# Kernel tuning notes

Hardware: AMD Instinct MI355X
Metric: run time of the kernel (lower is better)

Reference implementation:

```python
import jax, jax.numpy as jnp
import numpy as np

B, S, D, H = 16, 512, 768, 8
DK = D // H
MAXREL = 128
VOCAB = 30000


def setup_inputs() -> dict:
    key = jax.random.key(0)
    ks = jax.random.split(key, 20)
    p = lambda i, shape: (jax.random.normal(ks[i], shape, dtype=jnp.float32) * 0.02)
    return {
        "inputs": jax.random.normal(ks[0], (B, S, D), dtype=jnp.float32),
        "tok": jax.random.randint(ks[1], (B, S), 0, VOCAB),
        "seq_lens": S,
        "Wq": p(2, (D, D)), "bq": jnp.zeros((D,), jnp.float32),
        "Wk": p(3, (D, D)), "bk": jnp.zeros((D,), jnp.float32),
        "rel_emb": p(4, (2 * MAXREL + 1, DK)),
        "W0": p(5, (D, D)), "b0": jnp.zeros((D,), jnp.float32),
        "W1": p(6, (D, D)), "b1": jnp.zeros((D,), jnp.float32),
        "scale_w": jnp.ones((2,), jnp.float32) / 2.0,
        "Wf": p(7, (D, D)), "bf": jnp.zeros((D,), jnp.float32),
        "Wfc": p(8, (2 * D, D)), "bfc": jnp.zeros((D,), jnp.float32),
        "Wg": p(9, (D, D)), "bg": jnp.zeros((D,), jnp.float32),
    }


def reference(inputs, tok, seq_lens, Wq, bq, Wk, bk, rel_emb, W0, b0, W1, b1,
              scale_w, Wf, bf, Wfc, bfc, Wg, bg):
    b, s, d = inputs.shape
    h = H
    dk = d // h
    scale = 1.0 / jnp.sqrt(jnp.asarray(dk, inputs.dtype))

    # projections -> (b, h, s, dk)
    q = (inputs @ Wq + bq).reshape(b, s, h, dk).transpose(0, 2, 1, 3)
    k = (inputs @ Wk + bk).reshape(b, s, h, dk).transpose(0, 2, 1, 3)

    scores = jnp.einsum('bhqd,bhkd->bhqk', q, k) * scale

    # relative position bias from head-mean query
    pos = jnp.arange(s)
    dist = jnp.clip(pos[None, :] - pos[:, None], -MAXREL, MAXREL) + MAXREL
    rel = rel_emb[dist]                          # (s, s, dk)
    q_mean = q.mean(axis=1)                      # (b, s, dk)
    rel_scores = jnp.einsum('bqd,qkd->bqk', q_mean, rel) * scale
    scores = scores + rel_scores[:, None]        # broadcast over heads

    key_mask = (tok != 0)[:, None, None, :]      # (b,1,1,s)
    scores = jnp.where(key_mask, scores, jnp.asarray(-1e9, scores.dtype))
    p_attn = jax.nn.softmax(scores, axis=-1)     # (b,h,s,s)

    # head-averaged adjacency with forced self-loops
    adj = p_attn.mean(axis=1)                    # (b,s,s)
    eye = jnp.eye(s, dtype=adj.dtype)
    adj = adj * (1.0 - eye) + eye
    mask_ = (tok != 0).astype(adj.dtype)[:, :seq_lens, None]  # (b,s,1)
    adj = mask_ * adj

    denom = adj.sum(axis=2, keepdims=True) + 1.0

    # dense GCN layers (dropout = identity at inference)
    out = inputs
    feats = []
    for Wl, bl in ((W0, b0), (W1, b1)):
        ax = adj @ out                           # (b,s,d)
        out = jax.nn.relu((ax @ Wl + bl) / denom)
        feats.append(out)

    # multi-scale fusion
    w = jax.nn.softmax(scale_w)
    combined = w[0] * feats[0] + w[1] * feats[1]
    x = combined @ Wf + bf

    # global context gating (pool over full sequence)
    g_avg = x.mean(axis=1)
    g_max = x.max(axis=1)
    gc = jnp.concatenate([g_avg, g_max], axis=-1) @ Wfc + bfc  # (b,d)
    gate = jax.nn.sigmoid(gc @ Wg + bg)                        # (b,d)
    outputs = x + gate[:, None, :] * gc[:, None, :]
    return (outputs, adj)
```

## Files before the change

kernel.cpp:

```cpp
#include <hip/hip_runtime.h>
#include <hip/hip_bf16.h>
#include <math.h>

#define Bc 16
#define Sc 512
#define Dc 768
#define Hc 8
#define DKc 96
#define MAXRELc 128
#define RBLD 384

typedef __attribute__((ext_vector_type(8))) short bf16x8;
typedef __attribute__((ext_vector_type(4))) float f32x4;

static __device__ __forceinline__ unsigned short f2b(float f) {
    __hip_bfloat16 h = __float2bfloat16(f);
    return *(unsigned short*)&h;
}
static __device__ __forceinline__ float b2f(unsigned short u) {
    union { float f; unsigned v; } x;
    x.v = ((unsigned)u) << 16;
    return x.f;
}

static __device__ __forceinline__ long long fl_off(int rowg, int d) {
    const int h = d / 96, rr = d % 96;
    const int ks = rr >> 5, lg = (rr >> 3) & 3, ii = rr & 7;
    return ((((long long)(rowg >> 4) * 8 + h) * 3 + ks) * 4 + lg) * 128 + (rowg & 15) * 8 + ii;
}

#if defined(__has_builtin)
#if __has_builtin(__builtin_amdgcn_global_load_lds)
#define HAS_GLLDS 1
#endif
#endif

#ifdef HAS_GLLDS
typedef __attribute__((address_space(1))) void as1_void;
typedef __attribute__((address_space(3))) void as3_void;
static __device__ __forceinline__ void gl_lds16(const void* g, void* l) {
    __builtin_amdgcn_global_load_lds((as1_void*)(unsigned long long)g,
                                     (as3_void*)(unsigned long long)l, 16, 0, 0);
}
#endif

#define SWS(row, lg) (((((lg) + ((row) >> 1)) & 3)) * 8)

__global__ __launch_bounds__(256) void cvt_bf16_kernel(const float* __restrict__ in,
                                                       unsigned short* __restrict__ out)
{
    const long long idx = ((long long)blockIdx.x * 256 + threadIdx.x) * 8;
    const float4 a = *(const float4*)(in + idx);
    const float4 b = *(const float4*)(in + idx + 4);
    bf16x8 v;
    v[0] = (short)f2b(a.x); v[1] = (short)f2b(a.y); v[2] = (short)f2b(a.z); v[3] = (short)f2b(a.w);
    v[4] = (short)f2b(b.x); v[5] = (short)f2b(b.y); v[6] = (short)f2b(b.z); v[7] = (short)f2b(b.w);
    *(bf16x8*)(out + idx) = v;
}

struct WT5 { const float* s[5]; unsigned short* d[5]; };

__global__ __launch_bounds__(256) void wtrans5_kernel(WT5 p)
{
    const float* W = p.s[blockIdx.z];
    unsigned short* Wt = p.d[blockIdx.z];
    __shared__ float td[64][65];
    const int n0 = blockIdx.x * 64, k0 = blockIdx.y * 64;
    const int t = threadIdx.x, r = t >> 2, c4 = (t & 3) * 16;
#pragma unroll
    for (int j = 0; j < 4; ++j) {
        const float4 v = *(const float4*)(W + (long long)(k0 + r) * Dc + n0 + c4 + j * 4);
        td[r][c4 + j * 4 + 0] = v.x;
        td[r][c4 + j * 4 + 1] = v.y;
        td[r][c4 + j * 4 + 2] = v.z;
        td[r][c4 + j * 4 + 3] = v.w;
    }
    __syncthreads();
    bf16x8 v0, v1;
#pragma unroll
    for (int i = 0; i < 8; ++i) {
        v0[i] = (short)f2b(td[c4 + i][r]);
        v1[i] = (short)f2b(td[c4 + 8 + i][r]);
    }
    unsigned short* dst = Wt + (long long)(n0 + r) * Dc + k0 + c4;
    *(bf16x8*)dst = v0;
    *(bf16x8*)(dst + 8) = v1;
}

__global__ __launch_bounds__(256) void catbias_kernel(const float* __restrict__ a,
                                                      const float* __restrict__ b,
                                                      float* __restrict__ o)
{
    const int i = blockIdx.x * 256 + threadIdx.x;
    o[i] = (i < Dc) ? a[i] : b[i - Dc];
}

__global__ __launch_bounds__(256) void atrans_kernel(const unsigned short* __restrict__ in,
                                                     unsigned short* __restrict__ outT)
{
    __shared__ unsigned short td[64][66];
    const int b = blockIdx.z, s0 = blockIdx.y * 64, n0 = blockIdx.x * 64;
    const int t = threadIdx.x, r = t >> 2, c = (t & 3) * 16;
    const unsigned short* src = in + ((long long)(b * Sc + s0 + r)) * Dc + n0 + c;
    *(bf16x8*)&td[r][c] = *(const bf16x8*)src;
    *(bf16x8*)&td[r][c + 8] = *(const bf16x8*)(src + 8);
    __syncthreads();
    bf16x8 v0, v1;
#pragma unroll
    for (int i = 0; i < 8; ++i) {
        v0[i] = (short)td[c + i][r];
        v1[i] = (short)td[c + 8 + i][r];
    }
    unsigned short* dst = outT + ((long long)b * Dc + n0 + r) * Sc + s0 + c;
    *(bf16x8*)dst = v0;
    *(bf16x8*)(dst + 8) = v1;
}

__global__ __launch_bounds__(256) void gemm_bf16(
    const unsigned short* __restrict__ A, const unsigned short* __restrict__ Bt,
    int K, int ldc, long long sA, long long sB, long long sC,
    const float* __restrict__ bias, const float* __restrict__ denom, int relu_flag,
    float* __restrict__ Cf, unsigned short* __restrict__ Cbf, float bscale,
    const unsigned short* __restrict__ comb_o1, const float* __restrict__ scale_w,
    int qk_mode, unsigned short* __restrict__ Kfl_out)
{
    const int bz = blockIdx.z;
    A  += (long long)bz * sA;
    Bt += (long long)bz * sB;
    const int row0 = blockIdx.y * 128, col0 = blockIdx.x * 64;

    __shared__ unsigned short Al[2][128 * 32];
    __shared__ unsigned short Bl[2][64 * 32];

    const int t = threadIdx.x;
    const int w = t >> 6, l = t & 63, lg = l >> 4, ll = l & 15;
    const int wr = (w >> 1) * 64, wc = (w & 1) * 32;

    f32x4 acc[4][2];
#pragma unroll
    for (int m = 0; m < 4; ++m)
#pragma unroll
        for (int n = 0; n < 2; ++n) acc[m][n] = (f32x4){0.f, 0.f, 0.f, 0.f};

    const int ksw = (((t & 3) - (t >> 3)) & 3) * 8;
    const unsigned short* Ag = A + (long long)(row0 + (t >> 2)) * K + ksw;
    const unsigned short* Bg = Bt + (long long)(col0 + (t >> 2)) * K + ksw;
    const long long halfA = 64LL * K;
    const int nt = K >> 5;

#ifdef HAS_GLLDS
    gl_lds16(Ag, &Al[0][t * 8]);
    gl_lds16(Ag + halfA, &Al[0][2048 + t * 8]);
    gl_lds16(Bg, &Bl[0][t * 8]);
    __syncthreads();
    int cur = 0;
    for (int tt = 0; tt < nt; ++tt) {
        if (tt + 1 < nt) {
            const int ko = (tt + 1) << 5;
            gl_lds16(Ag + ko, &Al[cur ^ 1][t * 8]);
            gl_lds16(Ag + halfA + ko, &Al[cur ^ 1][2048 + t * 8]);
            gl_lds16(Bg + ko, &Bl[cur ^ 1][t * 8]);
        }
        bf16x8 af[4], bv[2];
#pragma unroll
        for (int m = 0; m < 4; ++m) {
            const int row = wr + m * 16 + ll;
            af[m] = *(const bf16x8*)&Al[cur][row * 32 + SWS(row, lg)];
        }
#pragma unroll
        for (int n = 0; n < 2; ++n) {
            const int row = wc + n * 16 + ll;
            bv[n] = *(const bf16x8*)&Bl[cur][row * 32 + SWS(row, lg)];
        }
#pragma unroll
        for (int m = 0; m < 4; ++m)
#pragma unroll
            for (int n = 0; n < 2; ++n)
                acc[m][n] = __builtin_amdgcn_mfma_f32_16x16x32_bf16(af[m], bv[n], acc[m][n], 0, 0, 0);
        __syncthreads();
        cur ^= 1;
    }
#else
    for (int k0 = 0; k0 < K; k0 += 32) {
        const bf16x8 a0 = *(const bf16x8*)(Ag + k0);
        const bf16x8 a1 = *(const bf16x8*)(Ag + halfA + k0);
        const bf16x8 b0 = *(const bf16x8*)(Bg + k0);
        __syncthreads();
        *(bf16x8*)&Al[0][t * 8] = a0;
        *(bf16x8*)&Al[0][2048 + t * 8] = a1;
        *(bf16x8*)&Bl[0][t * 8] = b0;
        __syncthreads();
        bf16x8 af[4], bv[2];
#pragma unroll
        for (int m = 0; m < 4; ++m) {
            const int row = wr + m * 16 + ll;
            af[m] = *(const bf16x8*)&Al[0][row * 32 + SWS(row, lg)];
        }
#pragma unroll
        for (int n = 0; n < 2; ++n) {
            const int row = wc + n * 16 + ll;
            bv[n] = *(const bf16x8*)&Bl[0][row * 32 + SWS(row, lg)];
        }
#pragma unroll
        for (int m = 0; m < 4; ++m)
#pragma unroll
            for (int n = 0; n < 2; ++n)
                acc[m][n] = __builtin_amdgcn_mfma_f32_16x16x32_bf16(af[m], bv[n], acc[m][n], 0, 0, 0);
    }
#endif

    if (qk_mode) {
#pragma unroll
        for (int m = 0; m < 4; ++m) {
#pragma unroll
            for (int n = 0; n < 2; ++n) {
                const int colg = col0 + wc + n * 16 + ll;
                const int isQ = colg < Dc;
                const int d = isQ ? colg : colg - Dc;
                const float bvl = bias[colg];
#pragma unroll
                for (int r = 0; r < 4; ++r) {
                    const int rowg = row0 + wr + m * 16 + lg * 4 + r;
                    float v = acc[m][n][r] + bvl;
                    if (isQ) v *= bscale;
                    (isQ ? Cbf : Kfl_out)[fl_off(rowg, d)] = f2b(v);
                }
            }
        }
        return;
    }

    float w0c = 0.f, w1c = 0.f;
    if (comb_o1) {
        const float s0 = scale_w[0], s1 = scale_w[1];
        const float mx = fmaxf(s0, s1);
        const float e0 = __expf(s0 - mx), e1 = __expf(s1 - mx);
        w0c = e0 / (e0 + e1);
        w1c = e1 / (e0 + e1);
    }

#pragma unroll
    for (int m = 0; m < 4; ++m) {
#pragma unroll
        for (int n = 0; n < 2; ++n) {
            const int colg = col0 + wc + n * 16 + ll;
            const float bvl = bias ? bias[colg] : 0.f;
#pragma unroll
            for (int r = 0; r < 4; ++r) {
                const int rowg = row0 + wr + m * 16 + lg * 4 + r;
                float v = acc[m][n][r] + bvl;
                if (denom) v /= denom[rowg];
                if (relu_flag) v = fmaxf(v, 0.f);
                const long long off = (long long)bz * sC + (long long)rowg * ldc + colg;
                if (comb_o1) v = w0c * b2f(comb_o1[off]) + w1c * v;
                if (Cbf) Cbf[off] = f2b(v);
                if (Cf) Cf[off] = v;
            }
        }
    }
}

__global__ __launch_bounds__(256) void qmean_kernel(const unsigned short* __restrict__ Qfl,
                                                    unsigned short* __restrict__ qmbf)
{
    const int idx = blockIdx.x * 256 + threadIdx.x;
    const int bi = idx / DKc, k = idx % DKc;
    const int g = bi >> 4, llr = bi & 15;
    const int ks = k >> 5, lg = (k >> 3) & 3, ii = k & 7;
    float s = 0.f;
#pragma unroll
    for (int h = 0; h < Hc; ++h)
        s += b2f(Qfl[((((long long)g * 8 + h) * 3 + ks) * 4 + lg) * 128 + llr * 8 + ii]);
    qmbf[idx] = f2b(s * 0.125f);
}

__global__ __launch_bounds__(256) void relpad_kernel(const float* __restrict__ rel_emb,
                                                     unsigned short* __restrict__ relbf)
{
    const int idx = blockIdx.x * 256 + threadIdx.x;
    const int n = idx / DKc, k = idx % DKc;
    relbf[idx] = (n < 2 * MAXRELc + 1) ? f2b(rel_emb[n * DKc + k]) : (unsigned short)0;
}

__global__ __launch_bounds__(256) void adj_mfma_kernel(
    const unsigned short* __restrict__ Qfl, const unsigned short* __restrict__ Kfl,
    const int* __restrict__ tok, const unsigned short* __restrict__ rbb,
    float* __restrict__ adj_out, unsigned short* __restrict__ adjbf_out,
    float* __restrict__ denom_out)
{
    const int b  = blockIdx.x >> 5;
    const int i0 = (blockIdx.x & 31) << 4;
    const int tid = threadIdx.x;
    const int w  = tid >> 6;
    const int l  = tid & 63;
    const int lg = l >> 4;
    const int ll = l & 15;
    const int c0 = w << 7;

    __shared__ float red[4][16];

    const int tokbase = b * Sc;
    const int qg  = b * 32 + (i0 >> 4);
    const int kgb = b * 32 + w * 8;

    float bias[8][4];
    float adjacc[8][4];
#pragma unroll
    for (int f = 0; f < 8; ++f) {
        const int j = c0 + f * 16 + ll;
        const bool km = (tok[tokbase + j] == 0);
#pragma unroll
        for (int r = 0; r < 4; ++r) {
            const int i = i0 + lg * 4 + r;
            int dd = j - i;
            dd = dd < -MAXRELc ? -MAXRELc : (dd > MAXRELc ? MAXRELc : dd);
            bias[f][r] = km ? -1e9f
                            : b2f(rbb[(long long)(tokbase + i) * RBLD + dd + MAXRELc]);
            adjacc[f][r] = 0.f;
        }
    }

    for (int h = 0; h < Hc; ++h) {
        bf16x8 afr[3];
#pragma unroll
        for (int ks = 0; ks < 3; ++ks)
            afr[ks] = *(const bf16x8*)(Qfl + ((((long long)qg * 8 + h) * 3 + ks) << 9) + l * 8);

        float ex[8][4];
        float psum[4] = {0.f, 0.f, 0.f, 0.f};
#pragma unroll
        for (int f = 0; f < 8; ++f) {
            const long long kbase = (((long long)(kgb + f) * 8 + h) * 3) << 9;
            f32x4 acc = {0.f, 0.f, 0.f, 0.f};
#pragma unroll
            for (int ks = 0; ks < 3; ++ks) {
                const bf16x8 bfr = *(const bf16x8*)(Kfl + kbase + (ks << 9) + l * 8);
                acc = __builtin_amdgcn_mfma_f32_16x16x32_bf16(afr[ks], bfr, acc, 0, 0, 0);
            }
#pragma unroll
            for (int r = 0; r < 4; ++r) {
                const float e = __expf(acc[r] + bias[f][r]);
                ex[f][r] = e;
                psum[r] += e;
            }
        }
#pragma unroll
        for (int r = 0; r < 4; ++r) {
            psum[r] += __shfl_xor(psum[r], 1);
            psum[r] += __shfl_xor(psum[r], 2);
            psum[r] += __shfl_xor(psum[r], 4);
            psum[r] += __shfl_xor(psum[r], 8);
        }
        if (ll == 0) {
#pragma unroll
            for (int r = 0; r < 4; ++r) red[w][lg * 4 + r] = psum[r];
        }
        __syncthreads();
#pragma unroll
        for (int r = 0; r < 4; ++r) {
            const int rr = lg * 4 + r;
            const float s = red[0][rr] + red[1][rr] + red[2][rr] + red[3][rr];
            const float inv = 0.125f / s;
#pragma unroll
            for (int f = 0; f < 8; ++f) adjacc[f][r] += ex[f][r] * inv;
        }
        __syncthreads();
    }

    bool rowm[4];
#pragma unroll
    for (int r = 0; r < 4; ++r) rowm[r] = (tok[tokbase + i0 + lg * 4 + r] != 0);

    float psum[4] = {0.f, 0.f, 0.f, 0.f};
#pragma unroll
    for (int f = 0; f < 8; ++f) {
        const int j = c0 + f * 16 + ll;
#pragma unroll
        for (int r = 0; r < 4; ++r) {
            const int i = i0 + lg * 4 + r;
            float v = adjacc[f][r];
            if (j == i) v = 1.f;
            if (!rowm[r]) v = 0.f;
            const long long off = (long long)(tokbase + i) * Sc + j;
            adj_out[off] = v;
            adjbf_out[off] = f2b(v);
            psum[r] += v;
        }
    }
#pragma unroll
    for (int r = 0; r < 4; ++r) {
        psum[r] += __shfl_xor(psum[r], 1);
        psum[r] += __shfl_xor(psum[r], 2);
        psum[r] += __shfl_xor(psum[r], 4);
        psum[r] += __shfl_xor(psum[r], 8);
    }
    if (ll == 0) {
#pragma unroll
        for (int r = 0; r < 4; ++r) red[w][lg * 4 + r] = psum[r];
    }
    __syncthreads();
    if (w == 0 && ll == 0) {
#pragma unroll
        for (int r = 0; r < 4; ++r) {
            const int rr = lg * 4 + r;
            denom_out[tokbase + i0 + rr] =
                red[0][rr] + red[1][rr] + red[2][rr] + red[3][rr] + 1.f;
        }
    }
}

__global__ __launch_bounds__(256) void pool_part_kernel(const float* __restrict__ x,
                                                        float* __restrict__ psum,
                                                        float* __restrict__ pmax)
{
    const int b = blockIdx.z, ct = blockIdx.x, scn = blockIdx.y;
    const int t = threadIdx.x, c = ct * 64 + (t & 63), sg = t >> 6;
    float s = 0.f, m = -INFINITY;
#pragma unroll
    for (int si = 0; si < 16; ++si) {
        const int srow = scn * 64 + sg * 16 + si;
        const float v = x[((long long)(b * Sc + srow)) * Dc + c];
        s += v;
        m = fmaxf(m, v);
    }
    __shared__ float rs[4][64], rm[4][64];
    rs[sg][t & 63] = s;
    rm[sg][t & 63] = m;
    __syncthreads();
    if (t < 64) {
        s = rs[0][t] + rs[1][t] + rs[2][t] + rs[3][t];
        m = fmaxf(fmaxf(rm[0][t], rm[1][t]), fmaxf(rm[2][t], rm[3][t]));
        const long long o = ((long long)b * 8 + scn) * Dc + ct * 64 + t;
        psum[o] = s;
        pmax[o] = m;
    }
}

__global__ __launch_bounds__(256) void pool_red_kernel(const float* __restrict__ psum,
                                                       const float* __restrict__ pmax,
                                                       float* __restrict__ gpool)
{
    const int idx = blockIdx.x * 256 + threadIdx.x;
    const int b = idx / Dc, c = idx % Dc;
    float s = 0.f, m = -INFINITY;
#pragma unroll
    for (int i = 0; i < 8; ++i) {
        const long long o = ((long long)b * 8 + i) * Dc + c;
        s += psum[o];
        m = fmaxf(m, pmax[o]);
    }
    gpool[(long long)b * 1536 + c] = s * (1.f / Sc);
    gpool[(long long)b * 1536 + Dc + c] = m;
}

__global__ __launch_bounds__(256) void skinny_partial(const float* __restrict__ in,
                                                      const float* __restrict__ W,
                                                      float* __restrict__ part, int K)
{
    __shared__ float sin_[16][96];
    const int t = threadIdx.x;
    const int nt = blockIdx.x, kc = blockIdx.y;
    const int k0 = kc * 96;
    for (int idx = t; idx < 16 * 96; idx += 256) {
        const int b = idx / 96, c = idx % 96;
        sin_[b][c] = in[(long long)b * K + k0 + c];
    }
    __syncthreads();
    const int n = nt * 64 + (t & 63), kg = t >> 6;
    float acc[16];
#pragma unroll
    for (int b = 0; b < 16; ++b) acc[b] = 0.f;
    for (int kk = 0; kk < 24; ++kk) {
        const float wv = W[(long long)(k0 + kg * 24 + kk) * Dc + n];
#pragma unroll
        for (int b = 0; b < 16; ++b) acc[b] += sin_[b][kg * 24 + kk] * wv;
    }
    float* dst = part + ((long long)(kc * 4 + kg) * 16) * Dc + n;
#pragma unroll
    for (int b = 0; b < 16; ++b) dst[(long long)b * Dc] = acc[b];
}

__global__ __launch_bounds__(256) void skinny_reduce(const float* __restrict__ part,
                                                     const float* __restrict__ bias,
                                                     float* __restrict__ outp,
                                                     int nslices, int do_sigmoid)
{
    const int idx = blockIdx.x * 256 + threadIdx.x;
    const int n = idx % Dc;
    float s = bias[n];
    for (int i = 0; i < nslices; ++i) s += part[(long long)i * (16 * Dc) + idx];
    if (do_sigmoid) s = 1.f / (1.f + __expf(-s));
    outp[idx] = s;
}

__global__ __launch_bounds__(256) void final_kernel(const float* __restrict__ x,
                                                    const float* __restrict__ gate,
                                                    const float* __restrict__ gc,
                                                    float* __restrict__ outp)
{
    const long long idx = (long long)blockIdx.x * 256 + threadIdx.x;
    const int c = (int)(idx % Dc);
    const long long bs = idx / Dc;
    const int b = (int)(bs / Sc);
    outp[idx] = x[idx] + gate[b * Dc + c] * gc[b * Dc + c];
}

extern "C" void kernel_launch(void* const* d_in, const int* in_sizes, int n_in,
                              void* d_out, int out_size, void* d_ws, size_t ws_size,
                              hipStream_t stream)
{
    (void)in_sizes; (void)n_in; (void)out_size; (void)ws_size;

    const float* X       = (const float*)d_in[0];
    const int*   tok     = (const int*)d_in[1];
    const float* Wq      = (const float*)d_in[3];
    const float* bq      = (const float*)d_in[4];
    const float* Wk      = (const float*)d_in[5];
    const float* bk      = (const float*)d_in[6];
    const float* rel_emb = (const float*)d_in[7];
    const float* W0      = (const float*)d_in[8];
    const float* b0      = (const float*)d_in[9];
    const float* W1      = (const float*)d_in[10];
    const float* b1      = (const float*)d_in[11];
    const float* scale_w = (const float*)d_in[12];
    const float* Wf      = (const float*)d_in[13];
    const float* bf      = (const float*)d_in[14];
    const float* Wfc     = (const float*)d_in[15];
    const float* bfc     = (const float*)d_in[16];
    const float* Wg      = (const float*)d_in[17];
    const float* bg      = (const float*)d_in[18];

    float* outp = (float*)d_out;
    const long long NBSD = (long long)Bc * Sc * Dc;
    float* adj = outp + NBSD;

    char* wsb = (char*)d_ws;
    const long long MiB = 1048576LL;
    unsigned short* Xbf   = (unsigned short*)(wsb);
    unsigned short* rb_bf = (unsigned short*)(wsb);
    unsigned short* qmbf  = (unsigned short*)(wsb + 6 * MiB);
    unsigned short* relbf = (unsigned short*)(wsb + 8 * MiB);
    float* gpool   = (float*)(wsb);
    float* gcb     = (float*)(wsb + 128 * 1024);
    float* gate    = (float*)(wsb + 192 * 1024);
    float* poolsum = (float*)(wsb + 256 * 1024);
    float* poolmax = (float*)(wsb + 640 * 1024);
    float* pp1     = (float*)(wsb + 1 * MiB);
    float* pp2     = (float*)(wsb + 4 * MiB);
    unsigned short* Qfl    = (unsigned short*)(wsb + 12 * MiB);
    unsigned short* combbf = Qfl;
    unsigned short* Kfl    = (unsigned short*)(wsb + 24 * MiB);
    unsigned short* out1bf = Kfl;
    unsigned short* Xt    = (unsigned short*)(wsb + 36 * MiB);
    unsigned short* out1t = Xt;
    float*          xf    = (float*)(wsb + 36 * MiB);
    unsigned short* adjbf = (unsigned short*)(wsb + 48 * MiB);
    unsigned short* Wqt  = (unsigned short*)(wsb + 56 * MiB);
    unsigned short* Wkt  = (unsigned short*)(wsb + 56 * MiB + 1179648);
    unsigned short* axbf = (unsigned short*)(wsb + 56 * MiB);
    unsigned short* W0t = (unsigned short*)(wsb + 68 * MiB);
    unsigned short* W1t = (unsigned short*)(wsb + 68 * MiB + 1179648);
    unsigned short* Wft = (unsigned short*)(wsb + 68 * MiB + 2359296);
    float*          denom = (float*)(wsb + 68 * MiB + 3538944);
    float*          bqk   = (float*)(wsb + 68 * MiB + 3538944 + 32768);

    const float qscale = 0.10206207261596577f;

    auto gemm = [&](const unsigned short* A, const unsigned short* Bt, int M, int N, int K,
                    int ldc, long long sA, long long sB, long long sC, int batch,
                    const float* bias, const float* den, int relu,
                    float* Cf, unsigned short* Cbf, float bscale,
                    const unsigned short* comb_o1, const float* sw,
                    int qk_mode, unsigned short* Kfl_out) {
        dim3 grid(N / 64, M / 128, batch);
        gemm_bf16<<<grid, 256, 0, stream>>>(A, Bt, K, ldc, sA, sB, sC, bias, den, relu,
                                            Cf, Cbf, bscale, comb_o1, sw, qk_mode, Kfl_out);
    };

    cvt_bf16_kernel<<<(int)(NBSD / 2048), 256, 0, stream>>>(X, Xbf);
    WT5 wt;
    wt.s[0] = Wq;  wt.d[0] = Wqt;
    wt.s[1] = Wk;  wt.d[1] = Wkt;
    wt.s[2] = W0;  wt.d[2] = W0t;
    wt.s[3] = W1;  wt.d[3] = W1t;
    wt.s[4] = Wf;  wt.d[4] = Wft;
    wtrans5_kernel<<<dim3(12, 12, 5), 256, 0, stream>>>(wt);
    catbias_kernel<<<6, 256, 0, stream>>>(bq, bk, bqk);
    gemm(Xbf, Wqt, Bc * Sc, 2 * Dc, Dc, 0, 0, 0, 0, 1, bqk, nullptr, 0,
         nullptr, Qfl, qscale, nullptr, nullptr, 1, Kfl);
    atrans_kernel<<<dim3(12, 8, 16), 256, 0, stream>>>(Xbf, Xt);
    qmean_kernel<<<(Bc * Sc * DKc) / 256, 256, 0, stream>>>(Qfl, qmbf);
    relpad_kernel<<<(RBLD * DKc) / 256, 256, 0, stream>>>(rel_emb, relbf);
    gemm(qmbf, relbf, Bc * Sc, RBLD, DKc, RBLD, 0, 0, 0, 1, nullptr, nullptr, 0,
         nullptr, rb_bf, 1.f, nullptr, nullptr, 0, nullptr);
    adj_mfma_kernel<<<Bc * (Sc / 16), 256, 0, stream>>>(Qfl, Kfl, tok, rb_bf, adj, adjbf, denom);
    gemm(adjbf, Xt, Sc, Dc, Sc, Dc, (long long)Sc * Sc, (long long)Dc * Sc, (long long)Sc * Dc,
         Bc, nullptr, nullptr, 0, nullptr, axbf, 1.f, nullptr, nullptr, 0, nullptr);
    gemm(axbf, W0t, Bc * Sc, Dc, Dc, Dc, 0, 0, 0, 1, b0, denom, 1,
         nullptr, out1bf, 1.f, nullptr, nullptr, 0, nullptr);
    atrans_kernel<<<dim3(12, 8, 16), 256, 0, stream>>>(out1bf, out1t);
    gemm(adjbf, out1t, Sc, Dc, Sc, Dc, (long long)Sc * Sc, (long long)Dc * Sc, (long long)Sc * Dc,
         Bc, nullptr, nullptr, 0, nullptr, axbf, 1.f, nullptr, nullptr, 0, nullptr);
    gemm(axbf, W1t, Bc * Sc, Dc, Dc, Dc, 0, 0, 0, 1, b1, denom, 1,
         nullptr, combbf, 1.f, out1bf, scale_w, 0, nullptr);
    gemm(combbf, Wft, Bc * Sc, Dc, Dc, Dc, 0, 0, 0, 1, bf, nullptr, 0,
         xf, nullptr, 1.f, nullptr, nullptr, 0, nullptr);
    pool_part_kernel<<<dim3(12, 8, 16), 256, 0, stream>>>(xf, poolsum, poolmax);
    pool_red_kernel<<<(Bc * Dc) / 256, 256, 0, stream>>>(poolsum, poolmax, gpool);
    skinny_partial<<<dim3(12, 16), 256, 0, stream>>>(gpool, Wfc, pp1, 2 * Dc);
    skinny_reduce<<<(Bc * Dc) / 256, 256, 0, stream>>>(pp1, bfc, gcb, 64, 0);
    skinny_partial<<<dim3(12, 8), 256, 0, stream>>>(gcb, Wg, pp2, Dc);
    skinny_reduce<<<(Bc * Dc) / 256, 256, 0, stream>>>(pp2, bg, gate, 32, 1);
    final_kernel<<<(int)(NBSD / 256), 256, 0, stream>>>(xf, gate, gcb, outp);
}
```

Baseline: 420.8 us.

## Triple-buffer GEMM LDS loads with explicit waitcnt and remap workgroups across XCDs

Moves the bf16 GEMM's global-to-LDS pipeline from double to triple buffering, prefetching two k-tiles ahead. The loop now syncs with a manual vmcnt wait and barrier instead of trailing __syncthreads, so more load latency can overlap the MFMA work. It also remaps the linear workgroup index so consecutive tiles are spread across the 8 XCDs, aiming for better L2 locality. The cost is 50% more LDS per block, which may lower occupancy, and correctness now depends on hand-written waitcnt counts.

```diff
diff --git a/kernel.cpp b/kernel.cpp
--- a/kernel.cpp
+++ b/kernel.cpp
@@ -124,13 +124,21 @@
     const unsigned short* __restrict__ comb_o1, const float* __restrict__ scale_w,
     int qk_mode, unsigned short* __restrict__ Kfl_out)
 {
-    const int bz = blockIdx.z;
+    const int gx = gridDim.x, gy = gridDim.y;
+    const int nwg = gx * gy * gridDim.z;
+    int lin = (blockIdx.z * gy + blockIdx.y) * gx + blockIdx.x;
+    lin = (lin & 7) * (nwg >> 3) + (lin >> 3);
+    const int bx = lin % gx;
+    const int rem = lin / gx;
+    const int by = rem % gy;
+    const int bz = rem / gy;
+
     A  += (long long)bz * sA;
     Bt += (long long)bz * sB;
-    const int row0 = blockIdx.y * 128, col0 = blockIdx.x * 64;
-
-    __shared__ unsigned short Al[2][128 * 32];
-    __shared__ unsigned short Bl[2][64 * 32];
+    const int row0 = by * 128, col0 = bx * 64;
+
+    __shared__ unsigned short Al[3][128 * 32];
+    __shared__ unsigned short Bl[3][64 * 32];
 
     const int t = threadIdx.x;
     const int w = t >> 6, l = t & 63, lg = l >> 4, ll = l & 15;
@@ -152,14 +160,17 @@
     gl_lds16(Ag, &Al[0][t * 8]);
     gl_lds16(Ag + halfA, &Al[0][2048 + t * 8]);
     gl_lds16(Bg, &Bl[0][t * 8]);
-    __syncthreads();
-    int cur = 0;
+    if (nt > 1) {
+        gl_lds16(Ag + 32, &Al[1][t * 8]);
+        gl_lds16(Ag + halfA + 32, &Al[1][2048 + t * 8]);
+        gl_lds16(Bg + 32, &Bl[1][t * 8]);
+    }
     for (int tt = 0; tt < nt; ++tt) {
+        const int cur = tt % 3;
         if (tt + 1 < nt) {
-            const int ko = (tt + 1) << 5;
-            gl_lds16(Ag + ko, &Al[cur ^ 1][t * 8]);
-            gl_lds16(Ag + halfA + ko, &Al[cur ^ 1][2048 + t * 8]);
-            gl_lds16(Bg + ko, &Bl[cur ^ 1][t * 8]);
+            asm volatile("s_waitcnt vmcnt(3)\n\ts_barrier" ::: "memory");
+        } else {
+            asm volatile("s_waitcnt vmcnt(0)\n\ts_barrier" ::: "memory");
         }
         bf16x8 af[4], bv[2];
 #pragma unroll
@@ -172,13 +183,19 @@
             const int row = wc + n * 16 + ll;
             bv[n] = *(const bf16x8*)&Bl[cur][row * 32 + SWS(row, lg)];
         }
+        asm volatile("s_waitcnt lgkmcnt(0)" ::: "memory");
+        if (tt + 2 < nt) {
+            const int ko = (tt + 2) << 5;
+            const int nxt = (tt + 2) % 3;
+            gl_lds16(Ag + ko, &Al[nxt][t * 8]);
+            gl_lds16(Ag + halfA + ko, &Al[nxt][2048 + t * 8]);
+            gl_lds16(Bg + ko, &Bl[nxt][t * 8]);
+        }
 #pragma unroll
         for (int m = 0; m < 4; ++m)
 #pragma unroll
             for (int n = 0; n < 2; ++n)
                 acc[m][n] = __builtin_amdgcn_mfma_f32_16x16x32_bf16(af[m], bv[n], acc[m][n], 0, 0, 0);
-        __syncthreads();
-        cur ^= 1;
     }
 #else
     for (int k0 = 0; k0 < K; k0 += 32) {
```

Result: faster. 405.9 us (-3.6%).
